# Optimization experiments

Hardware: AMD Instinct MI355X
Metric: run time of the kernel (lower is better)

## Reference

```python
import jax, jax.numpy as jnp
import numpy as np

B, C, H, T, L = 128, 16, 9, 2048, 9  # batch, channels, sensors, time, decomp levels
TAU = 1.0

def _conv(x, w, pad):
    # x: [N,C,H,W], w: [O,I,kh,kw]
    return jax.lax.conv_general_dilated(x, w, (1, 1), pad,
                                        dimension_numbers=('NCHW', 'OIHW', 'NCHW'))

def _prelu(x, a):
    return jnp.where(x >= 0, x, a * x)

def _branch(z, w1, a, w2):
    # ReflectionPad2d((1,1,0,0)) -> Conv(1,3) -> PReLU -> Conv(1,1) -> Tanh
    z = jnp.pad(z, ((0, 0), (0, 0), (0, 0), (1, 1)), mode='reflect')
    z = _prelu(_conv(z, w1, [(0, 0), (0, 0)]), a)
    return jnp.tanh(_conv(z, w2, [(0, 0), (0, 0)]))


def setup_inputs() -> dict:
    key = jax.random.key(0)
    ks = jax.random.split(key, 24)
    n = lambda k, s, sc=0.05: jax.random.normal(k, s, dtype=jnp.float32) * sc
    u = jax.random.uniform(ks[1], (L, 2 * B, 2, 1, 1), dtype=jnp.float32,
                           minval=1e-6, maxval=1.0 - 1e-6)
    inp = {
        'x': jax.random.normal(ks[0], (B, 1, H, T), dtype=jnp.float32),
        'gumbel_noise': -jnp.log(-jnp.log(u)),
        # conv_in stem
        'Wc1': n(ks[2], (C, 1, 1, 33)), 'bc1': jnp.zeros((C,), jnp.float32),
        'bn1_g': jnp.ones((C,), jnp.float32), 'bn1_b': jnp.zeros((C,), jnp.float32),
        'a_c1': jnp.float32(0.25),
        'Wc2': n(ks[3], (C, C, 1, 3)), 'bc2': jnp.zeros((C,), jnp.float32),
        'bn2_g': jnp.ones((C,), jnp.float32), 'bn2_b': jnp.zeros((C,), jnp.float32),
        'a_c2': jnp.float32(0.25),
        # per-level lifting P/U branches
        'WP1': n(ks[4], (L, C, C, 1, 3)), 'aP': jnp.full((L,), 0.25, jnp.float32),
        'WP2': n(ks[5], (L, C, C, 1, 1)),
        'WU1': n(ks[6], (L, C, C, 1, 3)), 'aU': jnp.full((L,), 0.25, jnp.float32),
        'WU2': n(ks[7], (L, C, C, 1, 1)),
        # per-level gumble routing head (pooled -> 1x1 C->C -> PReLU -> 1x1 C->2 -> PReLU)
        'Wg1': n(ks[8], (L, C, C, 1, 1)), 'ag1': jnp.full((L,), 0.25, jnp.float32),
        'Wg2': n(ks[9], (L, 2, C, 1, 1)), 'ag2': jnp.full((L,), 0.25, jnp.float32),
    }
    return inp


def _forward(x, Wc1, bc1, bn1_g, bn1_b, a_c1, Wc2, bc2, bn2_g, bn2_b, a_c2,
             WP1, aP, WP2, WU1, aU, WU2, Wg1, ag1, Wg2, ag2, gumbel_noise):
    rs = lambda v: v.reshape(1, -1, 1, 1)
    # conv_in stem (BatchNorm in eval form with default running stats)
    x = _conv(x, Wc1, [(0, 0), (16, 16)]) + rs(bc1)
    x = _prelu(x * rs(bn1_g) + rs(bn1_b), a_c1)
    x = _conv(x, Wc2, [(0, 0), (1, 1)]) + rs(bc2)
    x = _prelu(x * rs(bn2_g) + rs(bn2_b), a_c2)  # [B,C,H,T]

    feats = []
    for i in range(L):
        even, odd = x[..., ::2], x[..., 1::2]
        # modified lifting: c = even + U(odd); d = odd - P(c)
        c = even + _branch(odd, WU1[i], aU[i], WU2[i])
        d = odd - _branch(c, WP1[i], aP[i], WP2[i])
        out = jnp.stack([c, d], axis=1)  # [B,2,C,H,t]
        t = out.shape[-1]
        # gumble_block_2D: pool each (low/high) slice to [2B,C,1,1]
        pooled = out.reshape(B * 2, C, H, t).mean(axis=(2, 3), keepdims=True)
        hm = _prelu(_conv(pooled, Wg1[i], [(0, 0), (0, 0)]), ag1[i])
        hm = _prelu(_conv(hm, Wg2[i], [(0, 0), (0, 0)]), ag2[i])  # [2B,2,1,1]
        s = jax.nn.softmax(hm, axis=1)
        m = jax.nn.softmax((s + gumbel_noise[i]) / TAU, axis=1)
        m = m.reshape(B, 2, 2, 1, 1)
        input_conv = out * m[:, :, 0][..., None]  # gated conv branch [B,2,C,H,t]
        input_res = out * m[:, :, 1][..., None]   # gated residual branch
        feats.append(input_res.mean(axis=-1))      # [B,2,C,H]
        x = input_conv[:, 0]                       # gated low-pass feeds next level
    return jnp.stack(feats, axis=-1)  # [B,2,C,H,L]


def reference(x, gumbel_noise, Wc1, bc1, bn1_g, bn1_b, a_c1, Wc2, bc2, bn2_g,
              bn2_b, a_c2, WP1, aP, WP2, WU1, aU, WU2, Wg1, ag1, Wg2, ag2):
    return _forward(x, Wc1, bc1, bn1_g, bn1_b, a_c1, Wc2, bc2, bn2_g, bn2_b,
                    a_c2, WP1, aP, WP2, WU1, aU, WU2, Wg1, ag1, Wg2, ag2,
                    gumbel_noise)
```

## Files before the change

kernel.cpp:

```cpp
#include <hip/hip_runtime.h>
#include <hip/hip_bf16.h>


#define CB 16
#define HH 9
#define TT0 2048
#define RS_SLOT 36864
#define LPITCH 20

__device__ __forceinline__ float ftanh(float x) {
    float e = __expf(2.f * x);
    return 1.f - 2.f / (e + 1.f);
}
__device__ __forceinline__ float fprelu(float v, float a) {
    return v >= 0.f ? v : a * v;
}
__device__ __forceinline__ void ld16(const float* p, float* v) {
#pragma unroll
    for (int q = 0; q < 4; ++q) {
        float4 f = *(const float4*)(p + 4 * q);
        v[4 * q] = f.x; v[4 * q + 1] = f.y; v[4 * q + 2] = f.z; v[4 * q + 3] = f.w;
    }
}
__device__ __forceinline__ void ld16s(const float* p, float* v) {
#pragma unroll
    for (int q = 0; q < 4; ++q) {
        float4 f = *(const float4*)(p + 4 * q);
        v[4 * q] = f.x; v[4 * q + 1] = f.y; v[4 * q + 2] = f.z; v[4 * q + 3] = f.w;
    }
}
__device__ __forceinline__ void st16(float* p, const float* v) {
#pragma unroll
    for (int q = 0; q < 4; ++q) {
        float4 f; f.x = v[4 * q]; f.y = v[4 * q + 1]; f.z = v[4 * q + 2]; f.w = v[4 * q + 3];
        *(float4*)(p + 4 * q) = f;
    }
}
__device__ __forceinline__ int refl(int u, int t) {
    return u < 0 ? -u : (u >= t ? 2 * t - 2 - u : u);
}

__device__ __forceinline__ void rowsum_reduce(const float* vals, float* rs, int tile,
                                              int b, int h, int sdx, int tid) {
    __shared__ float red[4 * CB];
    const int lane = tid & 63, wv = tid >> 6;
    __syncthreads();
#pragma unroll
    for (int cc = 0; cc < CB; ++cc) {
        float s = vals[cc];
#pragma unroll
        for (int off = 32; off >= 1; off >>= 1) s += __shfl_xor(s, off, 64);
        if (lane == cc) red[wv * CB + cc] = s;
    }
    __syncthreads();
    if (tid < CB) {
        float s = red[tid] + red[CB + tid] + red[2 * CB + tid] + red[3 * CB + tid];
        rs[(size_t)tile * RS_SLOT + ((size_t)(2 * b + sdx) * CB + tid) * HH + h] = s;
    }
}

__global__ void wtrans_kernel(const float* __restrict__ Wc1, const float* __restrict__ Wc2,
                              const float* __restrict__ WU1, const float* __restrict__ WU2,
                              const float* __restrict__ WP1, const float* __restrict__ WP2,
                              float* __restrict__ W)
{
    const int tid = threadIdx.x;
    for (int idx = tid; idx < 528; idx += 256) {
        int k = idx >> 4, cc = idx & 15;
        W[idx] = Wc1[cc * 33 + k];
    }
    for (int idx = tid; idx < 768; idx += 256) {
        int k = idx >> 8, c2 = (idx >> 4) & 15, cc = idx & 15;
        W[528 + idx] = Wc2[(cc * 16 + c2) * 3 + k];
    }
    for (int i = 0; i < 9; ++i) {
        float* base = W + 1296 + i * 2048;
        const float* wu1 = WU1 + i * 768;
        const float* wp1 = WP1 + i * 768;
        const float* wu2 = WU2 + i * 256;
        const float* wp2 = WP2 + i * 256;
        for (int idx = tid; idx < 768; idx += 256) {
            int k = idx >> 8, c2 = (idx >> 4) & 15, cc = idx & 15;
            base[idx]        = wu1[cc * 48 + c2 * 3 + k];
            base[1024 + idx] = wp1[cc * 48 + c2 * 3 + k];
        }
        {
            int idx = tid;
            if (idx < 256) {
                int c2 = idx >> 4, cc = idx & 15;
                base[768 + idx]  = wu2[cc * 16 + c2];
                base[1792 + idx] = wp2[cc * 16 + c2];
            }
        }
    }
}

__device__ __forceinline__ void compute_c(
    const float* __restrict__ xrow, int j, int t, float sm,
    const float* __restrict__ W1, const float* __restrict__ W2, float aU,
    float* cv, float* ow1)
{
    float accz[CB];
#pragma unroll
    for (int i = 0; i < CB; ++i) accz[i] = 0.f;
#pragma unroll
    for (int k = 0; k < 3; ++k) {
        int um = refl(j - 1 + k, t);
        float ow[CB];
        ld16(xrow + (size_t)(2 * um + 1) * CB, ow);
        if (k == 1) {
#pragma unroll
            for (int i = 0; i < CB; ++i) ow1[i] = ow[i];
        }
#pragma unroll
        for (int c2 = 0; c2 < CB; ++c2) {
            float o = ow[c2];
            const float* wp = W1 + (k * 16 + c2) * 16;
#pragma unroll
            for (int cc = 0; cc < CB; ++cc)
                accz[cc] = fmaf(wp[cc], o, accz[cc]);
        }
    }
#pragma unroll
    for (int i = 0; i < CB; ++i) accz[i] = fprelu(accz[i], aU);
    float bacc[CB];
#pragma unroll
    for (int cc = 0; cc < CB; ++cc) bacc[cc] = 0.f;
#pragma unroll
    for (int c2 = 0; c2 < CB; ++c2) {
        float z = accz[c2];
        const float* wp = W2 + c2 * 16;
#pragma unroll
        for (int cc = 0; cc < CB; ++cc)
            bacc[cc] = fmaf(wp[cc], z, bacc[cc]);
    }
    float ev[CB];
    ld16(xrow + (size_t)(2 * j) * CB, ev);
#pragma unroll
    for (int cc = 0; cc < CB; ++cc)
        cv[cc] = sm * ev[cc] + ftanh(sm * bacc[cc]);
}

__device__ __forceinline__ void compute_d_tanh(
    const float* __restrict__ ldc_base, int j, int t, int seg0,
    const float* __restrict__ W1, const float* __restrict__ W2, float aP,
    float* tv)
{
    float accz[CB];
#pragma unroll
    for (int i = 0; i < CB; ++i) accz[i] = 0.f;
#pragma unroll
    for (int k = 0; k < 3; ++k) {
        int um = refl(j - 1 + k, t);
        float cw[CB];
        ld16s(ldc_base + (seg0 + um) * LPITCH, cw);
#pragma unroll
        for (int c2 = 0; c2 < CB; ++c2) {
            float o = cw[c2];
            const float* wp = W1 + (k * 16 + c2) * 16;
#pragma unroll
            for (int cc = 0; cc < CB; ++cc)
                accz[cc] = fmaf(wp[cc], o, accz[cc]);
        }
    }
#pragma unroll
    for (int i = 0; i < CB; ++i) accz[i] = fprelu(accz[i], aP);
    float bacc[CB];
#pragma unroll
    for (int cc = 0; cc < CB; ++cc) bacc[cc] = 0.f;
#pragma unroll
    for (int c2 = 0; c2 < CB; ++c2) {
        float z = accz[c2];
        const float* wp = W2 + c2 * 16;
#pragma unroll
        for (int cc = 0; cc < CB; ++cc)
            bacc[cc] = fmaf(wp[cc], z, bacc[cc]);
    }
#pragma unroll
    for (int cc = 0; cc < CB; ++cc) tv[cc] = ftanh(bacc[cc]);
}

__global__ __launch_bounds__(256, 4) void front_kernel(
    const float* __restrict__ x, const float* __restrict__ Wt,
    const float* __restrict__ bc1,
    const float* __restrict__ bn1g, const float* __restrict__ bn1b,
    const float* __restrict__ ac1,
    const float* __restrict__ bc2,
    const float* __restrict__ bn2g, const float* __restrict__ bn2b,
    const float* __restrict__ ac2,
    float* __restrict__ y)
{
    const int tid = threadIdx.x;
    const int t0  = blockIdx.x * 254;
    const int h   = blockIdx.y;
    const int b   = blockIdx.z;
    const float* Wc1t = Wt;
    const float* Wc2t = Wt + 528;

    __shared__ float lds_x[288];
    __shared__ float lds_y[256 * LPITCH];

    const float* xrow = x + (size_t)(b * HH + h) * TT0;
    {
        int g = t0 - 17 + tid;
        lds_x[tid] = (g >= 0 && g < TT0) ? xrow[g] : 0.f;
        if (tid < 32) {
            int g2 = t0 + 239 + tid;
            lds_x[256 + tid] = (g2 >= 0 && g2 < TT0) ? xrow[g2] : 0.f;
        }
    }
    __syncthreads();

    const float a1 = ac1[0], a2 = ac2[0];
    float acc[CB];
#pragma unroll
    for (int cc = 0; cc < CB; ++cc) acc[cc] = bc1[cc];
#pragma unroll
    for (int k = 0; k < 33; ++k) {
        float xv = lds_x[tid + k];
        const float* wp = Wc1t + k * 16;
#pragma unroll
        for (int cc = 0; cc < CB; ++cc) acc[cc] = fmaf(wp[cc], xv, acc[cc]);
    }
#pragma unroll
    for (int cc = 0; cc < CB; ++cc)
        lds_y[tid * LPITCH + cc] = fprelu(acc[cc] * bn1g[cc] + bn1b[cc], a1);
    __syncthreads();

    const int jt = t0 + tid;
    if (tid < 254 && jt < TT0) {
        float acc2[CB];
#pragma unroll
        for (int cc = 0; cc < CB; ++cc) acc2[cc] = bc2[cc];
#pragma unroll
        for (int k = 0; k < 3; ++k) {
            int u = jt - 1 + k;
            if (u >= 0 && u < TT0) {
                float yv[CB];
                ld16s(&lds_y[(tid + k) * LPITCH], yv);
#pragma unroll
                for (int c2 = 0; c2 < CB; ++c2) {
                    float yvv = yv[c2];
                    const float* wp = Wc2t + (k * 16 + c2) * 16;
#pragma unroll
                    for (int cc = 0; cc < CB; ++cc)
                        acc2[cc] = fmaf(wp[cc], yvv, acc2[cc]);
                }
            }
        }
        float ov[CB];
#pragma unroll
        for (int cc = 0; cc < CB; ++cc) ov[cc] = fprelu(acc2[cc] * bn2g[cc] + bn2b[cc], a2);
        st16(y + ((size_t)(b * HH + h) * TT0 + jt) * CB, ov);
    }
}

__global__ __launch_bounds__(256, 2) void cd_kernel(
    const float* __restrict__ xin, float* __restrict__ xout,
    float* __restrict__ rs, const float* __restrict__ m0prev,
    const float* __restrict__ Wt,
    const float* __restrict__ aUp, const float* __restrict__ aPp, const int t)
{
    const int tid  = threadIdx.x;
    const int row  = blockIdx.x;
    const int tile = blockIdx.y;
    const int b = row / 9, h = row - 9 * b;
    const float sm = m0prev ? m0prev[b] : 1.f;
    const float aU = aUp[0], aP = aPp[0];
    const float* xrow = xin + (size_t)row * (2 * t) * CB;
    const int p0 = tile * 256;
    const int j = p0 + tid;
    const bool valid = (j < t);

    const float* WU1t = Wt;
    const float* WU2t = Wt + 768;
    const float* WP1t = Wt + 1024;
    const float* WP2t = Wt + 1792;

    __shared__ float ldc[258 * LPITCH];

    float cv[CB], ow1[CB];
#pragma unroll
    for (int i = 0; i < CB; ++i) { cv[i] = 0.f; ow1[i] = 0.f; }

    if (valid) {
        compute_c(xrow, j, t, sm, WU1t, WU2t, aU, cv, ow1);
        st16(&ldc[(tid + 1) * LPITCH], cv);
        st16(xout + ((size_t)row * t + j) * CB, cv);
    }
    if (tid < 2) {
        int jx = (tid == 0) ? p0 - 1 : p0 + 256;
        if (jx >= 0 && jx < t) {
            float hv[CB], dump[CB];
            compute_c(xrow, jx, t, sm, WU1t, WU2t, aU, hv, dump);
            st16(&ldc[(jx - p0 + 1) * LPITCH], hv);
        }
    }

    rowsum_reduce(cv, rs, tile, b, h, 0, tid);

    float dv[CB];
#pragma unroll
    for (int i = 0; i < CB; ++i) dv[i] = 0.f;

    if (valid) {
        float tv[CB];
        float accz[CB];
#pragma unroll
        for (int i = 0; i < CB; ++i) accz[i] = 0.f;
#pragma unroll
        for (int k = 0; k < 3; ++k) {
            int um = refl(j - 1 + k, t);
            int li = um - p0 + 1;
            float cw[CB];
            ld16s(&ldc[li * LPITCH], cw);
#pragma unroll
            for (int c2 = 0; c2 < CB; ++c2) {
                float o = cw[c2];
                const float* wp = WP1t + (k * 16 + c2) * 16;
#pragma unroll
                for (int cc = 0; cc < CB; ++cc)
                    accz[cc] = fmaf(wp[cc], o, accz[cc]);
            }
        }
#pragma unroll
        for (int i = 0; i < CB; ++i) accz[i] = fprelu(accz[i], aP);
        float bacc[CB];
#pragma unroll
        for (int cc = 0; cc < CB; ++cc) bacc[cc] = 0.f;
#pragma unroll
        for (int c2 = 0; c2 < CB; ++c2) {
            float z = accz[c2];
            const float* wp = WP2t + c2 * 16;
#pragma unroll
            for (int cc = 0; cc < CB; ++cc)
                bacc[cc] = fmaf(wp[cc], z, bacc[cc]);
        }
#pragma unroll
        for (int cc = 0; cc < CB; ++cc)
            dv[cc] = sm * ow1[cc] - ftanh(bacc[cc]);
        (void)tv;
    }
    rowsum_reduce(dv, rs, tile, b, h, 1, tid);
}

__global__ __launch_bounds__(256, 2) void cd_small_kernel(
    const float* __restrict__ xin, float* __restrict__ xout,
    float* __restrict__ rs, const float* __restrict__ m0prev,
    const float* __restrict__ Wt,
    const float* __restrict__ aUp, const float* __restrict__ aPp,
    const int t, const int log2t)
{
    const int tid  = threadIdx.x;
    const int j    = tid & (t - 1);
    const int rloc = tid >> log2t;
    const int row  = (blockIdx.x << (8 - log2t)) + rloc;
    const int b = row / 9, h = row - 9 * b;
    const float sm = m0prev[b];
    const float aU = aUp[0], aP = aPp[0];
    const float* xrow = xin + (size_t)row * (2 * t) * CB;

    const float* WU1t = Wt;
    const float* WU2t = Wt + 768;
    const float* WP1t = Wt + 1024;
    const float* WP2t = Wt + 1792;

    __shared__ float ldc[256 * LPITCH];

    float cv[CB], ow1[CB];
    compute_c(xrow, j, t, sm, WU1t, WU2t, aU, cv, ow1);
    st16(&ldc[tid * LPITCH], cv);
    st16(xout + ((size_t)row * t + j) * CB, cv);
    __syncthreads();

    float tv[CB];
    compute_d_tanh(ldc, j, t, rloc << log2t, WP1t, WP2t, aP, tv);
    float dv[CB];
#pragma unroll
    for (int cc = 0; cc < CB; ++cc) dv[cc] = sm * ow1[cc] - tv[cc];

#pragma unroll
    for (int cc = 0; cc < CB; ++cc) {
        float s = cv[cc];
        for (int off = t >> 1; off >= 1; off >>= 1) s += __shfl_xor(s, off, 64);
        cv[cc] = s;
        float s2 = dv[cc];
        for (int off = t >> 1; off >= 1; off >>= 1) s2 += __shfl_xor(s2, off, 64);
        dv[cc] = s2;
    }
    if (j == 0) {
#pragma unroll
        for (int cc = 0; cc < CB; ++cc) {
            rs[((size_t)(2 * b + 0) * CB + cc) * HH + h] = cv[cc];
            rs[((size_t)(2 * b + 1) * CB + cc) * HH + h] = dv[cc];
        }
    }
}

__global__ __launch_bounds__(192) void gate_kernel(
    const float* __restrict__ rs, const float* __restrict__ gn,
    const float* __restrict__ Wg1, const float* __restrict__ ag1p,
    const float* __restrict__ Wg2, const float* __restrict__ ag2p,
    float* __restrict__ out, float* __restrict__ m0buf,
    const int t, const int nt, const int li)
{
    const int bj  = blockIdx.x;
    const int tid = threadIdx.x;

    __shared__ float sums[144];
    __shared__ float sscale;

    if (tid < 144) {
        float s = 0.f;
        for (int tl = 0; tl < nt; ++tl)
            s += rs[(size_t)tl * RS_SLOT + (size_t)bj * 144 + tid];
        sums[tid] = s;
    }
    __syncthreads();

    if (tid == 0) {
        const float ag1 = ag1p[0], ag2 = ag2p[0];
        const float inv = 1.f / (9.f * (float)t);
        float pooled[CB];
#pragma unroll
        for (int cc = 0; cc < CB; ++cc) {
            float s = 0.f;
#pragma unroll
            for (int h = 0; h < HH; ++h) s += sums[cc * HH + h];
            pooled[cc] = s * inv;
        }
        float hm1[CB];
#pragma unroll
        for (int cc = 0; cc < CB; ++cc) {
            float s = 0.f;
#pragma unroll
            for (int c2 = 0; c2 < CB; ++c2) s = fmaf(Wg1[cc * CB + c2], pooled[c2], s);
            hm1[cc] = fprelu(s, ag1);
        }
        float h0 = 0.f, h1 = 0.f;
#pragma unroll
        for (int c2 = 0; c2 < CB; ++c2) {
            h0 = fmaf(Wg2[c2], hm1[c2], h0);
            h1 = fmaf(Wg2[CB + c2], hm1[c2], h1);
        }
        h0 = fprelu(h0, ag2); h1 = fprelu(h1, ag2);
        float mx = fmaxf(h0, h1);
        float e0 = __expf(h0 - mx), e1 = __expf(h1 - mx);
        float s0 = e0 / (e0 + e1), s1 = e1 / (e0 + e1);
        float a0 = s0 + gn[bj * 2 + 0], a1 = s1 + gn[bj * 2 + 1];
        float mx2 = fmaxf(a0, a1);
        float f0 = __expf(a0 - mx2), f1 = __expf(a1 - mx2);
        float m0 = f0 / (f0 + f1), m1 = f1 / (f0 + f1);
        sscale = m1 / (float)t;
        if ((bj & 1) == 0) m0buf[bj >> 1] = m0;
    }
    __syncthreads();

    if (tid < 144)
        out[(size_t)(bj * 144 + tid) * 9 + li] = sums[tid] * sscale;
}

extern "C" void kernel_launch(void* const* d_in, const int* in_sizes, int n_in,
                              void* d_out, int out_size, void* d_ws, size_t ws_size,
                              hipStream_t stream) {
    const float* x    = (const float*)d_in[0];
    const float* gn   = (const float*)d_in[1];
    const float* Wc1  = (const float*)d_in[2];
    const float* bc1  = (const float*)d_in[3];
    const float* bn1g = (const float*)d_in[4];
    const float* bn1b = (const float*)d_in[5];
    const float* ac1  = (const float*)d_in[6];
    const float* Wc2  = (const float*)d_in[7];
    const float* bc2  = (const float*)d_in[8];
    const float* bn2g = (const float*)d_in[9];
    const float* bn2b = (const float*)d_in[10];
    const float* ac2  = (const float*)d_in[11];
    const float* WP1  = (const float*)d_in[12];
    const float* aP   = (const float*)d_in[13];
    const float* WP2  = (const float*)d_in[14];
    const float* WU1  = (const float*)d_in[15];
    const float* aU   = (const float*)d_in[16];
    const float* WU2  = (const float*)d_in[17];
    const float* Wg1  = (const float*)d_in[18];
    const float* ag1  = (const float*)d_in[19];
    const float* Wg2  = (const float*)d_in[20];
    const float* ag2  = (const float*)d_in[21];
    float* out = (float*)d_out;

    char* ws = (char*)d_ws;
    const size_t sz0 = (size_t)128 * 9 * 2048 * 16 * 4;
    const size_t sz1 = sz0 / 2;
    float* buf0 = (float*)ws;
    float* buf1 = (float*)(ws + sz0);
    float* rs   = (float*)(ws + sz0 + sz1);
    float* m0b  = (float*)(ws + sz0 + sz1 + (size_t)4 * RS_SLOT * 4);
    float* wt   = (float*)(ws + sz0 + sz1 + (size_t)4 * RS_SLOT * 4 + 512);

    wtrans_kernel<<<1, 256, 0, stream>>>(Wc1, Wc2, WU1, WU2, WP1, WP2, wt);

    dim3 fgrid(9, 9, 128);
    front_kernel<<<fgrid, 256, 0, stream>>>(x, wt, bc1, bn1g, bn1b, ac1,
                                            bc2, bn2g, bn2b, ac2, buf0);

    float* cur = buf0;
    float* nxt = buf1;
    int t = 1024;
    for (int i = 0; i < 9; ++i) {
        const float* m0p = (i == 0) ? nullptr : m0b;
        const float* lw = wt + 1296 + i * 2048;
        int nt;
        if (t > 32) {
            nt = (t + 255) >> 8;
            dim3 lgrid(128 * 9, nt);
            cd_kernel<<<lgrid, 256, 0, stream>>>(cur, nxt, rs, m0p, lw,
                                                 aU + i, aP + i, t);
        } else {
            nt = 1;
            int log2t = 10 - i;
            int nblk = (1152 * t) >> 8;
            cd_small_kernel<<<nblk, 256, 0, stream>>>(cur, nxt, rs, m0b, lw,
                                                      aU + i, aP + i, t, log2t);
        }
        gate_kernel<<<256, 192, 0, stream>>>(
            rs, gn + i * 512, Wg1 + i * 256, ag1 + i, Wg2 + i * 32, ag2 + i,
            out, m0b, t, nt, i);
        float* tmp = cur; cur = nxt; nxt = tmp;
        t >>= 1;
    }
}
```

Measured before the change: 790.5 us.

## Fuse gating head into next level's lifting kernel and enlarge tiles

Removes the per-level gate_kernel launches by recomputing the Gumbel routing head inside the next level's cd kernel from the previous level's row sums, using ping-pong row-sum buffers. Only one final gate_kernel remains, for the last level. Each cd_kernel block now covers 512 time steps with two elements per thread, so there are fewer tiles and fewer halo recomputations, and the small-kernel threshold moves to t<128. The cost is redundant gate evaluation in every block and more shared memory per block.

```diff
diff --git a/kernel.cpp b/kernel.cpp
--- a/kernel.cpp
+++ b/kernel.cpp
@@ -40,6 +40,44 @@
     return u < 0 ? -u : (u >= t ? 2 * t - 2 - u : u);
 }
 
+__device__ __forceinline__ void gate_eval(
+    const float* __restrict__ g144, const float* __restrict__ Wg1,
+    float ag1, float ag2, const float* __restrict__ Wg2,
+    float inv, float gn0, float gn1, float* m0o, float* m1o)
+{
+    float pooled[CB];
+#pragma unroll
+    for (int cc = 0; cc < CB; ++cc) {
+        float s = 0.f;
+#pragma unroll
+        for (int h = 0; h < HH; ++h) s += g144[cc * HH + h];
+        pooled[cc] = s * inv;
+    }
+    float hm1[CB];
+#pragma unroll
+    for (int cc = 0; cc < CB; ++cc) {
+        float s = 0.f;
+#pragma unroll
+        for (int c2 = 0; c2 < CB; ++c2) s = fmaf(Wg1[cc * CB + c2], pooled[c2], s);
+        hm1[cc] = fprelu(s, ag1);
+    }
+    float h0 = 0.f, h1 = 0.f;
+#pragma unroll
+    for (int c2 = 0; c2 < CB; ++c2) {
+        h0 = fmaf(Wg2[c2], hm1[c2], h0);
+        h1 = fmaf(Wg2[CB + c2], hm1[c2], h1);
+    }
+    h0 = fprelu(h0, ag2); h1 = fprelu(h1, ag2);
+    float mx = fmaxf(h0, h1);
+    float e0 = __expf(h0 - mx), e1 = __expf(h1 - mx);
+    float s0 = e0 / (e0 + e1), s1 = e1 / (e0 + e1);
+    float a0 = s0 + gn0, a1 = s1 + gn1;
+    float mx2 = fmaxf(a0, a1);
+    float f0 = __expf(a0 - mx2), f1 = __expf(a1 - mx2);
+    *m0o = f0 / (f0 + f1);
+    *m1o = f1 / (f0 + f1);
+}
+
 __device__ __forceinline__ void rowsum_reduce(const float* vals, float* rs, int tile,
                                               int b, int h, int sdx, int tid) {
     __shared__ float red[4 * CB];
@@ -57,6 +95,7 @@
         float s = red[tid] + red[CB + tid] + red[2 * CB + tid] + red[3 * CB + tid];
         rs[(size_t)tile * RS_SLOT + ((size_t)(2 * b + sdx) * CB + tid) * HH + h] = s;
     }
+    __syncthreads();
 }
 
 __global__ void wtrans_kernel(const float* __restrict__ Wc1, const float* __restrict__ Wc2,
@@ -84,13 +123,10 @@
             base[idx]        = wu1[cc * 48 + c2 * 3 + k];
             base[1024 + idx] = wp1[cc * 48 + c2 * 3 + k];
         }
-        {
-            int idx = tid;
-            if (idx < 256) {
-                int c2 = idx >> 4, cc = idx & 15;
-                base[768 + idx]  = wu2[cc * 16 + c2];
-                base[1792 + idx] = wp2[cc * 16 + c2];
-            }
+        if (tid < 256) {
+            int c2 = tid >> 4, cc = tid & 15;
+            base[768 + tid]  = wu2[cc * 16 + c2];
+            base[1792 + tid] = wp2[cc * 16 + c2];
         }
     }
 }
@@ -257,39 +293,78 @@
 
 __global__ __launch_bounds__(256, 2) void cd_kernel(
     const float* __restrict__ xin, float* __restrict__ xout,
-    float* __restrict__ rs, const float* __restrict__ m0prev,
+    float* __restrict__ rs_out, const float* __restrict__ rs_prev,
     const float* __restrict__ Wt,
-    const float* __restrict__ aUp, const float* __restrict__ aPp, const int t)
+    const float* __restrict__ aUp, const float* __restrict__ aPp,
+    const float* __restrict__ gnp, const float* __restrict__ Wg1p,
+    const float* __restrict__ ag1p, const float* __restrict__ Wg2p,
+    const float* __restrict__ ag2p,
+    float* __restrict__ out, const int t, const int nt_prev, const int li_prev)
 {
     const int tid  = threadIdx.x;
     const int row  = blockIdx.x;
     const int tile = blockIdx.y;
     const int b = row / 9, h = row - 9 * b;
-    const float sm = m0prev ? m0prev[b] : 1.f;
     const float aU = aUp[0], aP = aPp[0];
     const float* xrow = xin + (size_t)row * (2 * t) * CB;
-    const int p0 = tile * 256;
-    const int j = p0 + tid;
-    const bool valid = (j < t);
+    const int p0 = tile * 512;
 
     const float* WU1t = Wt;
     const float* WU2t = Wt + 768;
     const float* WP1t = Wt + 1024;
     const float* WP2t = Wt + 1792;
 
-    __shared__ float ldc[258 * LPITCH];
-
-    float cv[CB], ow1[CB];
-#pragma unroll
-    for (int i = 0; i < CB; ++i) { cv[i] = 0.f; ow1[i] = 0.f; }
-
-    if (valid) {
-        compute_c(xrow, j, t, sm, WU1t, WU2t, aU, cv, ow1);
-        st16(&ldc[(tid + 1) * LPITCH], cv);
-        st16(xout + ((size_t)row * t + j) * CB, cv);
+    __shared__ float ldc[514 * LPITCH];
+    __shared__ float gsum[288];
+    __shared__ float shv[3];
+
+    float sm = 1.f;
+    if (rs_prev) {
+        const bool writer = (h == 0 && tile == 0);
+        const int nload = writer ? 288 : 144;
+        for (int idx = tid; idx < nload; idx += 256) {
+            float s = 0.f;
+            for (int sl = 0; sl < nt_prev; ++sl)
+                s += rs_prev[(size_t)sl * RS_SLOT + (size_t)b * 288 + idx];
+            gsum[idx] = s;
+        }
+        __syncthreads();
+        if (tid == 0 || (writer && tid == 1)) {
+            const float tp = 2.f * (float)t;
+            float m0, m1;
+            gate_eval(&gsum[tid * 144], Wg1p, ag1p[0], ag2p[0], Wg2p,
+                      1.f / (9.f * tp), gnp[(2 * b + tid) * 2 + 0],
+                      gnp[(2 * b + tid) * 2 + 1], &m0, &m1);
+            if (tid == 0) { shv[0] = m0; shv[1] = m1 / tp; }
+            else          { shv[2] = m1 / tp; }
+        }
+        __syncthreads();
+        sm = shv[0];
+        if (writer) {
+            float sc0 = shv[1], sc1 = shv[2];
+            for (int idx = tid; idx < 288; idx += 256)
+                out[(size_t)((size_t)b * 288 + idx) * 9 + li_prev] =
+                    gsum[idx] * (idx < 144 ? sc0 : sc1);
+        }
+    }
+
+    float sc[CB];
+#pragma unroll
+    for (int i = 0; i < CB; ++i) sc[i] = 0.f;
+#pragma unroll
+    for (int g = 0; g < 2; ++g) {
+        const int j = p0 + (g << 8) + tid;
+        if (j < t) {
+            float cv[CB], dump[CB];
+            compute_c(xrow, j, t, sm, WU1t, WU2t, aU, cv, dump);
+            st16(&ldc[(j - p0 + 1) * LPITCH], cv);
+            st16(xout + ((size_t)row * t + j) * CB, cv);
+#pragma unroll
+            for (int cc = 0; cc < CB; ++cc) sc[cc] += cv[cc];
+        }
     }
     if (tid < 2) {
-        int jx = (tid == 0) ? p0 - 1 : p0 + 256;
+        int jx = (tid == 0) ? p0 - 1 : p0 + 512;
         if (jx >= 0 && jx < t) {
             float hv[CB], dump[CB];
             compute_c(xrow, jx, t, sm, WU1t, WU2t, aU, hv, dump);
@@ -297,69 +372,60 @@
         }
     }
 
-    rowsum_reduce(cv, rs, tile, b, h, 0, tid);
-
-    float dv[CB];
-#pragma unroll
-    for (int i = 0; i < CB; ++i) dv[i] = 0.f;
-
-    if (valid) {
-        float tv[CB];
-        float accz[CB];
-#pragma unroll
-        for (int i = 0; i < CB; ++i) accz[i] = 0.f;
-#pragma unroll
-        for (int k = 0; k < 3; ++k) {
-            int um = refl(j - 1 + k, t);
-            int li = um - p0 + 1;
-            float cw[CB];
-            ld16s(&ldc[li * LPITCH], cw);
-#pragma unroll
-            for (int c2 = 0; c2 < CB; ++c2) {
-                float o = cw[c2];
-                const float* wp = WP1t + (k * 16 + c2) * 16;
-#pragma unroll
-                for (int cc = 0; cc < CB; ++cc)
-                    accz[cc] = fmaf(wp[cc], o, accz[cc]);
-            }
-        }
-#pragma unroll
-        for (int i = 0; i < CB; ++i) accz[i] = fprelu(accz[i], aP);
-        float bacc[CB];
-#pragma unroll
-        for (int cc = 0; cc < CB; ++cc) bacc[cc] = 0.f;
-#pragma unroll
-        for (int c2 = 0; c2 < CB; ++c2) {
-            float z = accz[c2];
-            const float* wp = WP2t + c2 * 16;
-#pragma unroll
-            for (int cc = 0; cc < CB; ++cc)
-                bacc[cc] = fmaf(wp[cc], z, bacc[cc]);
-        }
-#pragma unroll
-        for (int cc = 0; cc < CB; ++cc)
-            dv[cc] = sm * ow1[cc] - ftanh(bacc[cc]);
-        (void)tv;
-    }
-    rowsum_reduce(dv, rs, tile, b, h, 1, tid);
+    rowsum_reduce(sc, rs_out, tile, b, h, 0, tid);
+
+    float sd[CB];
+#pragma unroll
+    for (int i = 0; i < CB; ++i) sd[i] = 0.f;
+#pragma unroll
+    for (int g = 0; g < 2; ++g) {
+        const int j = p0 + (g << 8) + tid;
+        if (j < t) {
+            float tv[CB];
+            compute_d_tanh(ldc, j, t, 1 - p0, WP1t, WP2t, aP, tv);
+            float ov[CB];
+            ld16(xrow + (size_t)(2 * j + 1) * CB, ov);
+#pragma unroll
+            for (int cc = 0; cc < CB; ++cc) sd[cc] += sm * ov[cc] - tv[cc];
+        }
+    }
+    rowsum_reduce(sd, rs_out, tile, b, h, 1, tid);
 }
 
 __global__ __launch_bounds__(256, 2) void cd_small_kernel(
     const float* __restrict__ xin, float* __restrict__ xout,
-    float* __restrict__ rs, const float* __restrict__ m0prev,
+    float* __restrict__ rs_out, const float* __restrict__ rs_prev,
     const float* __restrict__ Wt,
     const float* __restrict__ aUp, const float* __restrict__ aPp,
-    const int t, const int log2t)
+    const float* __restrict__ gnp, const float* __restrict__ Wg1p,
+    const float* __restrict__ ag1p, const float* __restrict__ Wg2p,
+    const float* __restrict__ ag2p,
+    float* __restrict__ out, const int t, const int log2t, const int li_prev)
 {
     const int tid  = threadIdx.x;
     const int j    = tid & (t - 1);
     const int rloc = tid >> log2t;
     const int row  = (blockIdx.x << (8 - log2t)) + rloc;
     const int b = row / 9, h = row - 9 * b;
-    const float sm = m0prev[b];
     const float aU = aUp[0], aP = aPp[0];
+
+    const float* gp = rs_prev + (size_t)b * 288;
+    const float tp = 2.f * (float)t;
+    float m0, m1;
+    gate_eval(gp, Wg1p, ag1p[0], ag2p[0], Wg2p, 1.f / (9.f * tp),
+              gnp[(2 * b) * 2 + 0], gnp[(2 * b) * 2 + 1], &m0, &m1);
+    const float sm = m0;
+    if (h == 0) {
+        float m0x, m1x;
+        gate_eval(gp + 144, Wg1p, ag1p[0], ag2p[0], Wg2p, 1.f / (9.f * tp),
+                  gnp[(2 * b + 1) * 2 + 0], gnp[(2 * b + 1) * 2 + 1], &m0x, &m1x);
+        float sc0 = m1 / tp, sc1 = m1x / tp;
+        for (int idx = j; idx < 288; idx += t)
+            out[(size_t)((size_t)b * 288 + idx) * 9 + li_prev] =
+                gp[idx] * (idx < 144 ? sc0 : sc1);
+    }
+
     const float* xrow = xin + (size_t)row * (2 * t) * CB;
-
     const float* WU1t = Wt;
     const float* WU2t = Wt + 768;
     const float* WP1t = Wt + 1024;
@@ -391,8 +457,8 @@
     if (j == 0) {
 #pragma unroll
         for (int cc = 0; cc < CB; ++cc) {
-            rs[((size_t)(2 * b + 0) * CB + cc) * HH + h] = cv[cc];
-            rs[((size_t)(2 * b + 1) * CB + cc) * HH + h] = dv[cc];
+            rs_out[((size_t)(2 * b + 0) * CB + cc) * HH + h] = cv[cc];
+            rs_out[((size_t)(2 * b + 1) * CB + cc) * HH + h] = dv[cc];
         }
     }
 }
@@ -419,38 +485,9 @@
     __syncthreads();
 
     if (tid == 0) {
-        const float ag1 = ag1p[0], ag2 = ag2p[0];
-        const float inv = 1.f / (9.f * (float)t);
-        float pooled[CB];
-#pragma unroll
-        for (int cc = 0; cc < CB; ++cc) {
-            float s = 0.f;
-#pragma unroll
-            for (int h = 0; h < HH; ++h) s += sums[cc * HH + h];
-            pooled[cc] = s * inv;
-        }
-        float hm1[CB];
-#pragma unroll
-        for (int cc = 0; cc < CB; ++cc) {
-            float s = 0.f;
-#pragma unroll
-            for (int c2 = 0; c2 < CB; ++c2) s = fmaf(Wg1[cc * CB + c2], pooled[c2], s);
-            hm1[cc] = fprelu(s, ag1);
-        }
-        float h0 = 0.f, h1 = 0.f;
-#pragma unroll
-        for (int c2 = 0; c2 < CB; ++c2) {
-            h0 = fmaf(Wg2[c2], hm1[c2], h0);
-            h1 = fmaf(Wg2[CB + c2], hm1[c2], h1);
-        }
-        h0 = fprelu(h0, ag2); h1 = fprelu(h1, ag2);
-        float mx = fmaxf(h0, h1);
-        float e0 = __expf(h0 - mx), e1 = __expf(h1 - mx);
-        float s0 = e0 / (e0 + e1), s1 = e1 / (e0 + e1);
-        float a0 = s0 + gn[bj * 2 + 0], a1 = s1 + gn[bj * 2 + 1];
-        float mx2 = fmaxf(a0, a1);
-        float f0 = __expf(a0 - mx2), f1 = __expf(a1 - mx2);
-        float m0 = f0 / (f0 + f1), m1 = f1 / (f0 + f1);
+        float m0, m1;
+        gate_eval(sums, Wg1, ag1p[0], ag2p[0], Wg2, 1.f / (9.f * (float)t),
+                  gn[bj * 2 + 0], gn[bj * 2 + 1], &m0, &m1);
         sscale = m1 / (float)t;
         if ((bj & 1) == 0) m0buf[bj >> 1] = m0;
     }
@@ -490,11 +527,13 @@
     char* ws = (char*)d_ws;
     const size_t sz0 = (size_t)128 * 9 * 2048 * 16 * 4;
     const size_t sz1 = sz0 / 2;
+    const size_t rsz = (size_t)2 * RS_SLOT * 4;
     float* buf0 = (float*)ws;
     float* buf1 = (float*)(ws + sz0);
-    float* rs   = (float*)(ws + sz0 + sz1);
-    float* m0b  = (float*)(ws + sz0 + sz1 + (size_t)4 * RS_SLOT * 4);
-    float* wt   = (float*)(ws + sz0 + sz1 + (size_t)4 * RS_SLOT * 4 + 512);
+    float* rsA  = (float*)(ws + sz0 + sz1);
+    float* rsB  = (float*)(ws + sz0 + sz1 + rsz);
+    float* m0s  = (float*)(ws + sz0 + sz1 + 2 * rsz);
+    float* wt   = (float*)(ws + sz0 + sz1 + 2 * rsz + 512);
 
     wtrans_kernel<<<1, 256, 0, stream>>>(Wc1, Wc2, WU1, WU2, WP1, WP2, wt);
 
@@ -502,29 +541,35 @@
     front_kernel<<<fgrid, 256, 0, stream>>>(x, wt, bc1, bn1g, bn1b, ac1,
                                             bc2, bn2g, bn2b, ac2, buf0);
 
+    float* rsbuf[2] = {rsA, rsB};
     float* cur = buf0;
     float* nxt = buf1;
     int t = 1024;
     for (int i = 0; i < 9; ++i) {
-        const float* m0p = (i == 0) ? nullptr : m0b;
-        const float* lw = wt + 1296 + i * 2048;
-        int nt;
-        if (t > 32) {
-            nt = (t + 255) >> 8;
-            dim3 lgrid(128 * 9, nt);
-            cd_kernel<<<lgrid, 256, 0, stream>>>(cur, nxt, rs, m0p, lw,
-                                                 aU + i, aP + i, t);
+        float* rs_out = rsbuf[i & 1];
+        const float* rs_prev = (i == 0) ? nullptr : rsbuf[(i - 1) & 1];
+        const float* lw   = wt + 1296 + i * 2048;
+        const int ip      = (i >= 1) ? i - 1 : 0;
+        const float* gnp  = gn  + ip * 512;
+        const float* Wg1p = Wg1 + ip * 256;
+        const float* Wg2p = Wg2 + ip * 32;
+        const int nt_prev = (ip == 0) ? 2 : 1;
+        if (t >= 128) {
+            dim3 lgrid(128 * 9, (t + 511) >> 9);
+            cd_kernel<<<lgrid, 256, 0, stream>>>(
+                cur, nxt, rs_out, rs_prev, lw, aU + i, aP + i,
+                gnp, Wg1p, ag1 + ip, Wg2p, ag2 + ip, out, t, nt_prev, ip);
         } else {
-            nt = 1;
-            int log2t = 10 - i;
-            int nblk = (1152 * t) >> 8;
-            cd_small_kernel<<<nblk, 256, 0, stream>>>(cur, nxt, rs, m0b, lw,
-                                                      aU + i, aP + i, t, log2t);
-        }
-        gate_kernel<<<256, 192, 0, stream>>>(
-            rs, gn + i * 512, Wg1 + i * 256, ag1 + i, Wg2 + i * 32, ag2 + i,
-            out, m0b, t, nt, i);
+            int log2t = 31 - __builtin_clz(t);
+            int nblk  = (1152 * t) >> 8;
+            cd_small_kernel<<<nblk, 256, 0, stream>>>(
+                cur, nxt, rs_out, rs_prev, lw, aU + i, aP + i,
+                gnp, Wg1p, ag1 + ip, Wg2p, ag2 + ip, out, t, log2t, ip);
+        }
         float* tmp = cur; cur = nxt; nxt = tmp;
         t >>= 1;
     }
-}
+    gate_kernel<<<256, 192, 0, stream>>>(
+        rsbuf[0], gn + 8 * 512, Wg1 + 8 * 256, ag1 + 8, Wg2 + 8 * 32, ag2 + 8,
+        out, m0s, 4, 1, 8);
+}
```

Measured after the change: 855.3 us. 1.08x slower.
